# Optimization experiments

Hardware: AMD Instinct MI355X
Metric: run time of the kernel (lower is better)

The kernel has to match this reference:

```python
import jax, jax.numpy as jnp
import numpy as np

N_NODES = 100000
D_FEAT = 128
N_EDGES = 600000


def setup_inputs() -> dict:
    key = jax.random.key(0)
    k1, k2, k3 = jax.random.split(key, 3)
    z1 = jax.random.normal(k1, (N_NODES, D_FEAT), dtype=jnp.float32)
    z2 = jax.random.normal(k2, (N_NODES, D_FEAT), dtype=jnp.float32)
    edge_index = jax.random.randint(k3, (2, N_EDGES), 0, N_NODES, dtype=jnp.int64)
    return {"z1": z1, "z2": z2, "edge_index": edge_index}


def reference(z1, z2, edge_index):
    # Gather endpoint embeddings per edge, inner product, sigmoid.
    src = z1[edge_index[0]]  # [E, d]
    dst = z2[edge_index[1]]  # [E, d]
    logits = jnp.sum(src * dst, axis=1)  # [E]
    return jax.nn.sigmoid(logits)
```

## Files before the change

### kernel.cpp

```cpp
#include <hip/hip_runtime.h>
#include <hip/hip_bf16.h>
#include <math.h>


#define D_FEAT 128
#define LANES 32
#define EPG 4

__global__ __launch_bounds__(256) void ipd_kernel(
    const float* __restrict__ z1,
    const float* __restrict__ z2,
    const int* __restrict__ edge_index,
    float* __restrict__ out,
    int n_edges) {
  const int tid = blockIdx.x * blockDim.x + threadIdx.x;
  const int lane = tid & (LANES - 1);
  const int group = tid / LANES;
  const int ebase = group * EPG;
  if (ebase >= n_edges) return;

  const int4 s4 = *(const int4*)(edge_index + ebase);
  const int4 d4 = *(const int4*)(edge_index + n_edges + ebase);

  const int s[EPG] = {s4.x, s4.y, s4.z, s4.w};
  const int d[EPG] = {d4.x, d4.y, d4.z, d4.w};

  float4 va[EPG], vb[EPG];
#pragma unroll
  for (int i = 0; i < EPG; ++i) {
    va[i] = ((const float4*)(z1 + (size_t)s[i] * D_FEAT))[lane];
    vb[i] = ((const float4*)(z2 + (size_t)d[i] * D_FEAT))[lane];
  }

  float sum[EPG];
#pragma unroll
  for (int i = 0; i < EPG; ++i) {
    sum[i] = va[i].x * vb[i].x + va[i].y * vb[i].y +
             va[i].z * vb[i].z + va[i].w * vb[i].w;
  }

#pragma unroll
  for (int off = LANES / 2; off > 0; off >>= 1) {
#pragma unroll
    for (int i = 0; i < EPG; ++i) sum[i] += __shfl_xor(sum[i], off, LANES);
  }

  if (lane == 0) {
    float4 o;
    o.x = 1.0f / (1.0f + __expf(-sum[0]));
    o.y = 1.0f / (1.0f + __expf(-sum[1]));
    o.z = 1.0f / (1.0f + __expf(-sum[2]));
    o.w = 1.0f / (1.0f + __expf(-sum[3]));
    *(float4*)(out + ebase) = o;
  }
}

extern "C" void kernel_launch(void* const* d_in, const int* in_sizes, int n_in,
                              void* d_out, int out_size, void* d_ws, size_t ws_size,
                              hipStream_t stream) {
  const float* z1 = (const float*)d_in[0];
  const float* z2 = (const float*)d_in[1];
  const int* edge_index = (const int*)d_in[2];
  float* out = (float*)d_out;

  const int n_edges = in_sizes[2] / 2;

  const int block = 256;
  const int groups = (n_edges + EPG - 1) / EPG;
  const long long total_threads = (long long)groups * LANES;
  const int grid = (int)((total_threads + block - 1) / block);

  ipd_kernel<<<grid, block, 0, stream>>>(z1, z2, edge_index, out, n_edges);
}
```

Measured before the change: 178.2 us.

## Convert embeddings to fp16 in workspace before gathering edge dot products

Adds a pre-pass that converts z1 and z2 to half precision in the workspace. The gather kernel then reads 256-byte rows with 16 lanes per edge instead of 512-byte rows with 32 lanes, accumulating in fp32. This halves the gathered bytes, at the cost of an extra full read/write pass over both tensors on every call and reduced input precision. It falls back to the fp32 kernel when the workspace is too small.

```diff
diff --git a/kernel.cpp b/kernel.cpp
--- a/kernel.cpp
+++ b/kernel.cpp
@@ -1,27 +1,100 @@
 #include <hip/hip_runtime.h>
 #include <hip/hip_bf16.h>
+#include <hip/hip_fp16.h>
 #include <math.h>
 
 
 #define D_FEAT 128
-#define LANES 32
+
+__global__ __launch_bounds__(256) void convert_kernel(
+    const float* __restrict__ z1, const float* __restrict__ z2,
+    __half* __restrict__ z1h, __half* __restrict__ z2h, int n8) {
+  const int i = blockIdx.x * blockDim.x + threadIdx.x;
+  const int which = (i < n8) ? 0 : 1;
+  const int j = which ? (i - n8) : i;
+  if (i >= 2 * n8) return;
+  const float* src = which ? z2 : z1;
+  __half* dst = which ? z2h : z1h;
+
+  const float4* p = (const float4*)src + 2 * (size_t)j;
+  const float4 a = p[0];
+  const float4 b = p[1];
+  union { __half2 h[4]; float4 f; } u;
+  u.h[0] = __floats2half2_rn(a.x, a.y);
+  u.h[1] = __floats2half2_rn(a.z, a.w);
+  u.h[2] = __floats2half2_rn(b.x, b.y);
+  u.h[3] = __floats2half2_rn(b.z, b.w);
+  ((float4*)dst)[j] = u.f;
+}
+
+#define LANES_H 16
 #define EPG 4
 
-__global__ __launch_bounds__(256) void ipd_kernel(
-    const float* __restrict__ z1,
-    const float* __restrict__ z2,
-    const int* __restrict__ edge_index,
-    float* __restrict__ out,
-    int n_edges) {
+__global__ __launch_bounds__(256) void ipd_h_kernel(
+    const __half* __restrict__ z1h, const __half* __restrict__ z2h,
+    const int* __restrict__ edge_index, float* __restrict__ out, int n_edges) {
   const int tid = blockIdx.x * blockDim.x + threadIdx.x;
-  const int lane = tid & (LANES - 1);
-  const int group = tid / LANES;
+  const int lane = tid & (LANES_H - 1);
+  const int group = tid / LANES_H;
   const int ebase = group * EPG;
   if (ebase >= n_edges) return;
 
   const int4 s4 = *(const int4*)(edge_index + ebase);
   const int4 d4 = *(const int4*)(edge_index + n_edges + ebase);
+  const int s[EPG] = {s4.x, s4.y, s4.z, s4.w};
+  const int d[EPG] = {d4.x, d4.y, d4.z, d4.w};
 
+  float4 va[EPG], vb[EPG];
+#pragma unroll
+  for (int i = 0; i < EPG; ++i) {
+    va[i] = ((const float4*)(z1h + (size_t)s[i] * D_FEAT))[lane];
+    vb[i] = ((const float4*)(z2h + (size_t)d[i] * D_FEAT))[lane];
+  }
+
+  float sum[EPG];
+#pragma unroll
+  for (int i = 0; i < EPG; ++i) {
+    const __half2* ha = (const __half2*)&va[i];
+    const __half2* hb = (const __half2*)&vb[i];
+    float acc = 0.f;
+#pragma unroll
+    for (int k = 0; k < 4; ++k) {
+      const float2 fa = __half22float2(ha[k]);
+      const float2 fb = __half22float2(hb[k]);
+      acc += fa.x * fb.x + fa.y * fb.y;
+    }
+    sum[i] = acc;
+  }
+
+#pragma unroll
+  for (int off = LANES_H / 2; off > 0; off >>= 1) {
+#pragma unroll
+    for (int i = 0; i < EPG; ++i) sum[i] += __shfl_xor(sum[i], off, LANES_H);
+  }
+
+  if (lane == 0) {
+    float4 o;
+    o.x = 1.0f / (1.0f + __expf(-sum[0]));
+    o.y = 1.0f / (1.0f + __expf(-sum[1]));
+    o.z = 1.0f / (1.0f + __expf(-sum[2]));
+    o.w = 1.0f / (1.0f + __expf(-sum[3]));
+    *(float4*)(out + ebase) = o;
+  }
+}
+
+#define LANES_F 32
+
+__global__ __launch_bounds__(256) void ipd_f_kernel(
+    const float* __restrict__ z1, const float* __restrict__ z2,
+    const int* __restrict__ edge_index, float* __restrict__ out, int n_edges) {
+  const int tid = blockIdx.x * blockDim.x + threadIdx.x;
+  const int lane = tid & (LANES_F - 1);
+  const int group = tid / LANES_F;
+  const int ebase = group * EPG;
+  if (ebase >= n_edges) return;
+
+  const int4 s4 = *(const int4*)(edge_index + ebase);
+  const int4 d4 = *(const int4*)(edge_index + n_edges + ebase);
   const int s[EPG] = {s4.x, s4.y, s4.z, s4.w};
   const int d[EPG] = {d4.x, d4.y, d4.z, d4.w};
 
@@ -34,15 +107,14 @@
 
   float sum[EPG];
 #pragma unroll
-  for (int i = 0; i < EPG; ++i) {
+  for (int i = 0; i < EPG; ++i)
     sum[i] = va[i].x * vb[i].x + va[i].y * vb[i].y +
              va[i].z * vb[i].z + va[i].w * vb[i].w;
-  }
 
 #pragma unroll
-  for (int off = LANES / 2; off > 0; off >>= 1) {
+  for (int off = LANES_F / 2; off > 0; off >>= 1) {
 #pragma unroll
-    for (int i = 0; i < EPG; ++i) sum[i] += __shfl_xor(sum[i], off, LANES);
+    for (int i = 0; i < EPG; ++i) sum[i] += __shfl_xor(sum[i], off, LANES_F);
   }
 
   if (lane == 0) {
@@ -64,11 +136,28 @@
   float* out = (float*)d_out;
 
   const int n_edges = in_sizes[2] / 2;
+  const int n_feat_elems = in_sizes[0];
+
+  const size_t half_bytes = (size_t)n_feat_elems * sizeof(__half);
 
   const int block = 256;
-  const int groups = (n_edges + EPG - 1) / EPG;
-  const long long total_threads = (long long)groups * LANES;
-  const int grid = (int)((total_threads + block - 1) / block);
 
-  ipd_kernel<<<grid, block, 0, stream>>>(z1, z2, edge_index, out, n_edges);
+  if (ws_size >= 2 * half_bytes && (n_feat_elems % 8) == 0) {
+    __half* z1h = (__half*)d_ws;
+    __half* z2h = (__half*)((char*)d_ws + half_bytes);
+
+    const int n8 = n_feat_elems / 8;
+    const int cgrid = (2 * n8 + block - 1) / block;
+    convert_kernel<<<cgrid, block, 0, stream>>>(z1, z2, z1h, z2h, n8);
+
+    const int groups = (n_edges + EPG - 1) / EPG;
+    const long long total = (long long)groups * LANES_H;
+    const int grid = (int)((total + block - 1) / block);
+    ipd_h_kernel<<<grid, block, 0, stream>>>(z1h, z2h, edge_index, out, n_edges);
+  } else {
+    const int groups = (n_edges + EPG - 1) / EPG;
+    const long long total = (long long)groups * LANES_F;
+    const int grid = (int)((total + block - 1) / block);
+    ipd_f_kernel<<<grid, block, 0, stream>>>(z1, z2, edge_index, out, n_edges);
+  }
 }
```

New measurement: 168.6 us. 1.06x faster.
